# Kernel optimization log

Measured on AMD Instinct MI355X. Metric: run time of the kernel, lower is better.

The kernel has to match this reference:

```python
import jax, jax.numpy as jnp
import numpy as np

N_NODES = 100000
N_EDGES = 1600000
IN_DIM, HID, OUT = 128, 128, 64


def setup_inputs() -> dict:
    key = jax.random.key(0)
    ks = jax.random.split(key, 8)
    x = jax.random.normal(ks[0], (N_NODES, IN_DIM), dtype=jnp.float32)
    edge_index = jax.random.randint(ks[1], (2, N_EDGES), 0, N_NODES, dtype=jnp.int64)
    # Glorot-ish init for GCNConv linear weights (stored as [in, out]).
    W1 = jax.random.normal(ks[2], (IN_DIM, HID), dtype=jnp.float32) * (1.0 / np.sqrt(IN_DIM))
    b1 = jnp.zeros((HID,), dtype=jnp.float32)
    W2 = jax.random.normal(ks[3], (HID, HID), dtype=jnp.float32) * (1.0 / np.sqrt(HID))
    b2 = jnp.zeros((HID,), dtype=jnp.float32)
    W3 = jax.random.normal(ks[4], (HID, OUT), dtype=jnp.float32) * (1.0 / np.sqrt(HID))
    b3 = jnp.zeros((OUT,), dtype=jnp.float32)
    return {"x": x, "W1": W1, "b1": b1, "W2": W2, "b2": b2,
            "W3": W3, "b3": b3, "edge_index": edge_index}


def _gcn_norm(edge_index, num_nodes):
    # GCNConv default: add self loops, symmetric normalization D^{-1/2} A D^{-1/2}.
    loops = jnp.arange(num_nodes, dtype=edge_index.dtype)
    src = jnp.concatenate([edge_index[0], loops])
    dst = jnp.concatenate([edge_index[1], loops])
    deg = jax.ops.segment_sum(jnp.ones_like(dst, dtype=jnp.float32), dst,
                              num_segments=num_nodes)
    dinv = jnp.where(deg > 0, jax.lax.rsqrt(deg), 0.0)
    norm = dinv[src] * dinv[dst]  # [E + N]
    return src, dst, norm


def _gcn_conv(h, W, b, src, dst, norm, num_nodes):
    h = h @ W                                   # transform first (PyG GCNConv)
    msg = h[src] * norm[:, None]                # gather + scale
    agg = jax.ops.segment_sum(msg, dst, num_segments=num_nodes)  # scatter-add
    return agg + b


def _dropout(h, key, p=0.5):
    keep = jax.random.bernoulli(key, 1.0 - p, h.shape)
    return jnp.where(keep, h / (1.0 - p), 0.0)


def reference(x, W1, b1, W2, b2, W3, b3, edge_index):
    num_nodes = x.shape[0]
    src, dst, norm = _gcn_norm(edge_index, num_nodes)
    kd1, kd2 = jax.random.split(jax.random.key(42))
    h = jax.nn.relu(_gcn_conv(x, W1, b1, src, dst, norm, num_nodes))
    h = _dropout(h, kd1)
    h = jax.nn.relu(_gcn_conv(h, W2, b2, src, dst, norm, num_nodes))
    h = _dropout(h, kd2)
    return _gcn_conv(h, W3, b3, src, dst, norm, num_nodes)
```

## Files before the change

### kernel.cpp

```cpp
#include <hip/hip_runtime.h>
#include <stdint.h>

#define NN 100000
#define NE 1600000
#define NMASKW 400000

typedef float f4 __attribute__((ext_vector_type(4)));
typedef float f2 __attribute__((ext_vector_type(2)));
typedef unsigned short us4 __attribute__((ext_vector_type(4)));
typedef short s16x8 __attribute__((ext_vector_type(8)));

__device__ inline float bf2f(unsigned short u) {
  return __uint_as_float(((uint32_t)u) << 16);
}
__device__ inline unsigned short f2bf(float f) {
  uint32_t u = __float_as_uint(f);
  return (unsigned short)((u + 0x7fffu + ((u >> 16) & 1u)) >> 16);
}
__device__ inline float lo16(uint32_t q) { return __uint_as_float(q << 16); }
__device__ inline float hi16(uint32_t q) { return __uint_as_float(q & 0xffff0000u); }

__host__ __device__ inline void threefry2x32(uint32_t k0, uint32_t k1,
                                             uint32_t x0, uint32_t x1,
                                             uint32_t* y0, uint32_t* y1) {
  uint32_t ks[3] = {k0, k1, k0 ^ k1 ^ 0x1BD11BDAu};
  x0 += ks[0]; x1 += ks[1];
  const uint32_t R[2][4] = {{13u, 15u, 26u, 6u}, {17u, 29u, 16u, 24u}};
#pragma unroll
  for (int i = 0; i < 5; ++i) {
#pragma unroll
    for (int j = 0; j < 4; ++j) {
      uint32_t r = R[i & 1][j];
      x0 += x1;
      x1 = (x1 << r) | (x1 >> (32u - r));
      x1 ^= x0;
    }
    x0 += ks[(i + 1) % 3];
    x1 += ks[(i + 2) % 3] + (uint32_t)(i + 1);
  }
  *y0 = x0; *y1 = x1;
}

__device__ inline uint32_t tf_bits32(uint32_t k0, uint32_t k1, uint32_t idx) {
  uint32_t a, b;
  threefry2x32(k0, k1, 0u, idx, &a, &b);
  return a ^ b;
}

__global__ __launch_bounds__(256) void k_mask(uint32_t* __restrict__ m1,
                                              uint32_t* __restrict__ m2,
                                              uint32_t k10, uint32_t k11,
                                              uint32_t k20, uint32_t k21) {
  int t = blockIdx.x * 256 + threadIdx.x;
  if (t >= NMASKW) return;
  uint32_t base = (uint32_t)t * 32u;
  uint32_t w1 = 0, w2 = 0;
#pragma unroll 4
  for (int j = 0; j < 32; ++j) {
    w1 |= (tf_bits32(k10, k11, base + j) >> 31) << j;
    w2 |= (tf_bits32(k20, k21, base + j) >> 31) << j;
  }
  m1[t] = w1;
  m2[t] = w2;
}

__global__ void k_init(uint32_t* cnt) {
  int i = blockIdx.x * 256 + threadIdx.x;
  if (i < NN) cnt[i] = 0u;
}

__global__ void k_hist(const int* __restrict__ ei, uint32_t* __restrict__ cnt,
                       int* __restrict__ slot) {
  int e = blockIdx.x * 256 + threadIdx.x;
  if (e < NE) {
    int d = ei[NE + e];
    slot[e] = (int)atomicAdd(&cnt[d], 1u);
  }
}

__global__ void k_dinv(const uint32_t* __restrict__ cnt, float* __restrict__ dinv) {
  int i = blockIdx.x * 256 + threadIdx.x;
  if (i < NN) dinv[i] = 1.0f / sqrtf((float)(cnt[i] + 1u));
}

__global__ __launch_bounds__(256) void k_scan1(const uint32_t* __restrict__ cnt,
                                               uint32_t* __restrict__ rp,
                                               uint32_t* __restrict__ bsum) {
  __shared__ uint32_t sh[256];
  int t = threadIdx.x;
  int base = blockIdx.x * 1024 + t * 4;
  uint32_t v[4];
  uint32_t s = 0;
#pragma unroll
  for (int i = 0; i < 4; ++i) {
    int idx = base + i;
    v[i] = (idx < NN) ? cnt[idx] : 0u;
    s += v[i];
  }
  sh[t] = s;
  __syncthreads();
  for (int off = 1; off < 256; off <<= 1) {
    uint32_t x = sh[t];
    if (t >= off) x += sh[t - off];
    __syncthreads();
    sh[t] = x;
    __syncthreads();
  }
  uint32_t run = (t > 0) ? sh[t - 1] : 0u;
  if (t == 255) bsum[blockIdx.x] = sh[255];
#pragma unroll
  for (int i = 0; i < 4; ++i) {
    int idx = base + i;
    if (idx < NN) rp[idx] = run;
    run += v[i];
  }
}

__global__ void k_scan2(uint32_t* bsum, int nb) {
  if (threadIdx.x == 0 && blockIdx.x == 0) {
    uint32_t s = 0;
    for (int i = 0; i < nb; ++i) { uint32_t x = bsum[i]; bsum[i] = s; s += x; }
  }
}

__global__ void k_scan3(uint32_t* rp, const uint32_t* __restrict__ bsum) {
  int i = blockIdx.x * 256 + threadIdx.x;
  if (i < NN) rp[i] += bsum[i >> 10];
  if (i == 0) rp[NN] = (uint32_t)NE;
}

__global__ void k_scatter(const int* __restrict__ ei,
                          const uint32_t* __restrict__ rp,
                          const int* __restrict__ slot,
                          const float* __restrict__ dinv,
                          uint2* __restrict__ e2) {
  int e = blockIdx.x * 256 + threadIdx.x;
  if (e < NE) {
    int s = ei[e];
    int d = ei[NE + e];
    float w = dinv[s] * dinv[d];
    uint32_t pos = rp[d] + (uint32_t)slot[e];
    uint2 rec;
    rec.x = (uint32_t)s;
    rec.y = __float_as_uint(w);
    e2[pos] = rec;
  }
}

__global__ void k_wsplit(const float* __restrict__ W, int dout,
                         unsigned short* __restrict__ H,
                         unsigned short* __restrict__ L) {
  int lane = threadIdx.x;
  int kk = blockIdx.x & 3;
  int ct = blockIdx.x >> 2;
  int kbase = kk * 32 + (lane >> 4) * 8;
  int col = ct * 16 + (lane & 15);
  us4 h0, h1, l0, l1;
#pragma unroll
  for (int j = 0; j < 4; ++j) {
    float v = W[(size_t)(kbase + j) * dout + col];
    h0[j] = f2bf(v);
    l0[j] = f2bf(v - bf2f(h0[j]));
    float v2 = W[(size_t)(kbase + 4 + j) * dout + col];
    h1[j] = f2bf(v2);
    l1[j] = f2bf(v2 - bf2f(h1[j]));
  }
  size_t o = ((size_t)blockIdx.x * 64 + lane) * 8;
  *(us4*)(H + o) = h0; *(us4*)(H + o + 4) = h1;
  *(us4*)(L + o) = l0; *(us4*)(L + o + 4) = l1;
}

__global__ __launch_bounds__(256) void k_gemm1(
    const float* __restrict__ A, const unsigned short* __restrict__ Wh,
    const unsigned short* __restrict__ Wl, unsigned short* __restrict__ C) {
  constexpr int NT = 8;
  const int w = threadIdx.x >> 6;
  const int lane = threadIdx.x & 63;
  const int row0 = blockIdx.x * 64 + w * 16;
  int ar = row0 + (lane & 15);
  if (ar >= NN) ar = NN - 1;
  const int aoff = (lane >> 4) * 8;
  s16x8 afh[4], afl[4];
#pragma unroll
  for (int kk = 0; kk < 4; ++kk) {
    f4 v0 = *(const f4*)(A + (size_t)ar * 128 + kk * 32 + aoff);
    f4 v1 = *(const f4*)(A + (size_t)ar * 128 + kk * 32 + aoff + 4);
#pragma unroll
    for (int j = 0; j < 4; ++j) {
      unsigned short h = f2bf(v0[j]);
      afh[kk][j] = (short)h;
      afl[kk][j] = (short)f2bf(v0[j] - bf2f(h));
      unsigned short h2 = f2bf(v1[j]);
      afh[kk][j + 4] = (short)h2;
      afl[kk][j + 4] = (short)f2bf(v1[j] - bf2f(h2));
    }
  }
  f4 acc[NT];
#pragma unroll
  for (int t = 0; t < NT; ++t) acc[t] = (f4){0.f, 0.f, 0.f, 0.f};
#pragma unroll
  for (int ct = 0; ct < NT; ++ct) {
#pragma unroll
    for (int kk = 0; kk < 4; ++kk) {
      size_t bo = ((size_t)(ct * 4 + kk) * 64 + lane) * 8;
      s16x8 bh = *(const s16x8*)(Wh + bo);
      s16x8 bl = *(const s16x8*)(Wl + bo);
      acc[ct] = __builtin_amdgcn_mfma_f32_16x16x32_bf16(afh[kk], bh, acc[ct], 0, 0, 0);
      acc[ct] = __builtin_amdgcn_mfma_f32_16x16x32_bf16(afh[kk], bl, acc[ct], 0, 0, 0);
      acc[ct] = __builtin_amdgcn_mfma_f32_16x16x32_bf16(afl[kk], bh, acc[ct], 0, 0, 0);
    }
  }
  const int rbase = row0 + (lane >> 4) * 4;
  const int cbase = lane & 15;
#pragma unroll
  for (int ct = 0; ct < NT; ++ct) {
#pragma unroll
    for (int r = 0; r < 4; ++r) {
      int gr = rbase + r;
      if (gr < NN) C[(size_t)gr * 128 + ct * 16 + cbase] = f2bf(acc[ct][r]);
    }
  }
}

template <int DOUT>
__global__ __launch_bounds__(256) void k_gemm_mfma(
    const unsigned short* __restrict__ Ah, const unsigned short* __restrict__ Al,
    const unsigned short* __restrict__ Wh, const unsigned short* __restrict__ Wl,
    unsigned short* __restrict__ C) {
  constexpr int NT = DOUT / 16;
  const int w = threadIdx.x >> 6;
  const int lane = threadIdx.x & 63;
  const int row0 = blockIdx.x * 64 + w * 16;
  int ar = row0 + (lane & 15);
  if (ar >= NN) ar = NN - 1;
  const int aoff = (lane >> 4) * 8;
  s16x8 afh[4], afl[4];
#pragma unroll
  for (int kk = 0; kk < 4; ++kk) {
    afh[kk] = *(const s16x8*)(Ah + (size_t)ar * 128 + kk * 32 + aoff);
    afl[kk] = *(const s16x8*)(Al + (size_t)ar * 128 + kk * 32 + aoff);
  }
  f4 acc[NT];
#pragma unroll
  for (int t = 0; t < NT; ++t) acc[t] = (f4){0.f, 0.f, 0.f, 0.f};
#pragma unroll
  for (int ct = 0; ct < NT; ++ct) {
#pragma unroll
    for (int kk = 0; kk < 4; ++kk) {
      size_t bo = ((size_t)(ct * 4 + kk) * 64 + lane) * 8;
      s16x8 bh = *(const s16x8*)(Wh + bo);
      s16x8 bl = *(const s16x8*)(Wl + bo);
      acc[ct] = __builtin_amdgcn_mfma_f32_16x16x32_bf16(afh[kk], bh, acc[ct], 0, 0, 0);
      acc[ct] = __builtin_amdgcn_mfma_f32_16x16x32_bf16(afh[kk], bl, acc[ct], 0, 0, 0);
      acc[ct] = __builtin_amdgcn_mfma_f32_16x16x32_bf16(afl[kk], bh, acc[ct], 0, 0, 0);
    }
  }
  const int rbase = row0 + (lane >> 4) * 4;
  const int cbase = lane & 15;
#pragma unroll
  for (int ct = 0; ct < NT; ++ct) {
#pragma unroll
    for (int r = 0; r < 4; ++r) {
      int gr = rbase + r;
      if (gr < NN) C[(size_t)gr * DOUT + ct * 16 + cbase] = f2bf(acc[ct][r]);
    }
  }
}

__global__ __launch_bounds__(256) void k_agg_mid(
    const unsigned short* __restrict__ hb, const uint32_t* __restrict__ rp,
    const uint2* __restrict__ e2, const float* __restrict__ dinv,
    const float* __restrict__ bias, const uint32_t* __restrict__ mask,
    unsigned short* __restrict__ oh, unsigned short* __restrict__ ol) {
  int wid = __builtin_amdgcn_readfirstlane(blockIdx.x * 4 + (threadIdx.x >> 6));
  if (wid >= NN) return;
  const int lane = threadIdx.x & 63;
  const uint32_t beg = rp[wid], end = rp[wid + 1];
  const float dv = dinv[wid];
  const float sn = dv * dv;
  const char* hbase = (const char*)hb;
  float a0 = 0.f, a1 = 0.f, c0 = 0.f, c1 = 0.f;
  uint32_t u = beg;
  for (; u + 8 <= end; u += 8) {
    uint2 r[8];
#pragma unroll
    for (int i = 0; i < 8; ++i) r[i] = e2[u + i];
    uint32_t q[8];
#pragma unroll
    for (int i = 0; i < 8; ++i)
      q[i] = ((const uint32_t*)(hbase + ((size_t)r[i].x << 8)))[lane];
#pragma unroll
    for (int i = 0; i < 8; ++i) {
      float w = __uint_as_float(r[i].y);
      if (i & 1) {
        c0 = fmaf(w, lo16(q[i]), c0);
        c1 = fmaf(w, hi16(q[i]), c1);
      } else {
        a0 = fmaf(w, lo16(q[i]), a0);
        a1 = fmaf(w, hi16(q[i]), a1);
      }
    }
  }
  for (; u < end; ++u) {
    uint2 r = e2[u];
    uint32_t q = ((const uint32_t*)(hbase + ((size_t)r.x << 8)))[lane];
    float w = __uint_as_float(r.y);
    a0 = fmaf(w, lo16(q), a0);
    a1 = fmaf(w, hi16(q), a1);
  }
  a0 += c0; a1 += c1;
  uint32_t qs = ((const uint32_t*)(hbase + ((size_t)(uint32_t)wid << 8)))[lane];
  f2 bv = *(const f2*)(bias + lane * 2);
  a0 = fmaf(sn, lo16(qs), a0) + bv[0];
  a1 = fmaf(sn, hi16(qs), a1) + bv[1];
  a0 = fmaxf(a0, 0.f);
  a1 = fmaxf(a1, 0.f);
  uint32_t mw = mask[(uint32_t)wid * 4u + (uint32_t)(lane >> 4)];
  uint32_t b = (uint32_t)((lane & 15) * 2);
  a0 = ((mw >> b) & 1u) ? 0.f : a0 * 2.f;
  a1 = ((mw >> (b + 1u)) & 1u) ? 0.f : a1 * 2.f;
  unsigned short h0 = f2bf(a0), h1 = f2bf(a1);
  unsigned short g0 = f2bf(a0 - bf2f(h0)), g1 = f2bf(a1 - bf2f(h1));
  ((uint32_t*)oh)[(size_t)wid * 64 + lane] = (uint32_t)h0 | ((uint32_t)h1 << 16);
  ((uint32_t*)ol)[(size_t)wid * 64 + lane] = (uint32_t)g0 | ((uint32_t)g1 << 16);
}

__global__ __launch_bounds__(256) void k_agg_final(
    const unsigned short* __restrict__ hb, const uint32_t* __restrict__ rp,
    const uint2* __restrict__ e2, const float* __restrict__ dinv,
    const float* __restrict__ bias, float* __restrict__ out) {
  int wid = __builtin_amdgcn_readfirstlane(blockIdx.x * 4 + (threadIdx.x >> 6));
  if (wid >= NN) return;
  const int lane = threadIdx.x & 63;
  const uint32_t beg = rp[wid], end = rp[wid + 1];
  const float dv = dinv[wid];
  const float sn = dv * dv;
  const char* hbase = (const char*)hb;
  float a0 = 0.f, c0 = 0.f, a2 = 0.f, c2 = 0.f;
  uint32_t u = beg;
  for (; u + 8 <= end; u += 8) {
    uint2 r[8];
#pragma unroll
    for (int i = 0; i < 8; ++i) r[i] = e2[u + i];
    uint32_t q[8];
#pragma unroll
    for (int i = 0; i < 8; ++i)
      q[i] = (uint32_t)((const unsigned short*)(hbase + ((size_t)r[i].x << 7)))[lane];
#pragma unroll
    for (int i = 0; i < 8; ++i) {
      float w = __uint_as_float(r[i].y);
      float hv = __uint_as_float(q[i] << 16);
      if ((i & 3) == 0) a0 = fmaf(w, hv, a0);
      else if ((i & 3) == 1) c0 = fmaf(w, hv, c0);
      else if ((i & 3) == 2) a2 = fmaf(w, hv, a2);
      else c2 = fmaf(w, hv, c2);
    }
  }
  for (; u < end; ++u) {
    uint2 r = e2[u];
    uint32_t q = (uint32_t)((const unsigned short*)(hbase + ((size_t)r.x << 7)))[lane];
    a0 = fmaf(__uint_as_float(r.y), __uint_as_float(q << 16), a0);
  }
  a0 += c0 + a2 + c2;
  uint32_t qs = (uint32_t)((const unsigned short*)(hbase + ((size_t)(uint32_t)wid << 7)))[lane];
  a0 = fmaf(sn, __uint_as_float(qs << 16), a0) + bias[lane];
  out[(size_t)wid * 64 + lane] = a0;
}

extern "C" void kernel_launch(void* const* d_in, const int* in_sizes, int n_in,
                              void* d_out, int out_size, void* d_ws, size_t ws_size,
                              hipStream_t stream) {
  (void)in_sizes; (void)n_in; (void)out_size; (void)ws_size;
  const float* x  = (const float*)d_in[0];
  const float* W1 = (const float*)d_in[1];
  const float* b1 = (const float*)d_in[2];
  const float* W2 = (const float*)d_in[3];
  const float* b2 = (const float*)d_in[4];
  const float* W3 = (const float*)d_in[5];
  const float* b3 = (const float*)d_in[6];
  const int* ei   = (const int*)d_in[7];
  float* out = (float*)d_out;

  char* p = (char*)d_ws;
  auto alloc = [&](size_t bytes) -> void* {
    void* r = (void*)p;
    p += (bytes + 255) & ~(size_t)255;
    return r;
  };
  uint32_t* cnt  = (uint32_t*)alloc((size_t)NN * 4);
  float*    dinv = (float*)alloc((size_t)NN * 4);
  uint32_t* rp   = (uint32_t*)alloc((size_t)(NN + 1) * 4);
  uint32_t* bsum = (uint32_t*)alloc(1024);
  int*      slot = (int*)alloc((size_t)NE * 4);
  uint2*    e2   = (uint2*)alloc((size_t)NE * 8);
  uint32_t* m1   = (uint32_t*)alloc((size_t)NMASKW * 4);
  uint32_t* m2   = (uint32_t*)alloc((size_t)NMASKW * 4);
  unsigned short* ah = (unsigned short*)alloc((size_t)NN * 128 * 2);
  unsigned short* al = (unsigned short*)alloc((size_t)NN * 128 * 2);
  unsigned short* hb = (unsigned short*)alloc((size_t)NN * 128 * 2);
  unsigned short* w1h = (unsigned short*)alloc(32 * 64 * 8 * 2);
  unsigned short* w1l = (unsigned short*)alloc(32 * 64 * 8 * 2);
  unsigned short* w2h = (unsigned short*)alloc(32 * 64 * 8 * 2);
  unsigned short* w2l = (unsigned short*)alloc(32 * 64 * 8 * 2);
  unsigned short* w3h = (unsigned short*)alloc(16 * 64 * 8 * 2);
  unsigned short* w3l = (unsigned short*)alloc(16 * 64 * 8 * 2);

  uint32_t kd1a, kd1b, kd2a, kd2b;
  threefry2x32(0u, 42u, 0u, 0u, &kd1a, &kd1b);
  threefry2x32(0u, 42u, 0u, 1u, &kd2a, &kd2b);

  const int gbN = (NN + 255) / 256;
  const int gbE = (NE + 255) / 256;
  const int gbScan = (NN + 1023) / 1024;
  const int gbGemm = (NN + 63) / 64;
  const int gbAgg = (NN + 3) / 4;
  const int gbMask = (NMASKW + 255) / 256;

  k_init<<<gbN, 256, 0, stream>>>(cnt);
  k_hist<<<gbE, 256, 0, stream>>>(ei, cnt, slot);
  k_dinv<<<gbN, 256, 0, stream>>>(cnt, dinv);
  k_scan1<<<gbScan, 256, 0, stream>>>(cnt, rp, bsum);
  k_scan2<<<1, 64, 0, stream>>>(bsum, gbScan);
  k_scan3<<<gbN, 256, 0, stream>>>(rp, bsum);
  k_scatter<<<gbE, 256, 0, stream>>>(ei, rp, slot, dinv, e2);

  k_mask<<<gbMask, 256, 0, stream>>>(m1, m2, kd1a, kd1b, kd2a, kd2b);
  k_wsplit<<<32, 64, 0, stream>>>(W1, 128, w1h, w1l);
  k_wsplit<<<32, 64, 0, stream>>>(W2, 128, w2h, w2l);
  k_wsplit<<<16, 64, 0, stream>>>(W3, 64, w3h, w3l);

  k_gemm1<<<gbGemm, 256, 0, stream>>>(x, w1h, w1l, hb);
  k_agg_mid<<<gbAgg, 256, 0, stream>>>(hb, rp, e2, dinv, b1, m1, ah, al);
  k_gemm_mfma<128><<<gbGemm, 256, 0, stream>>>(ah, al, w2h, w2l, hb);
  k_agg_mid<<<gbAgg, 256, 0, stream>>>(hb, rp, e2, dinv, b2, m2, ah, al);
  k_gemm_mfma<64><<<gbGemm, 256, 0, stream>>>(ah, al, w3h, w3l, hb);
  k_agg_final<<<gbAgg, 256, 0, stream>>>(hb, rp, e2, dinv, b3, out);
}
```

Measured before the change: 440.9 us.

## Fuse setup kernels and split edges across quarter-waves in aggregation

Merges the histogram and dropout-mask kernels into one interleaved launch, folds dinv into the scan, replaces the init kernel with a memset, and merges the three weight-split launches into one. The aggregation kernels now handle four edges at once per wave, with each 16-lane group doing 16-byte row gathers, followed by a cross-group shuffle reduction. This cuts launch count and issues fewer, wider gathers per edge. The cost is shuffle reduction overhead and padded tail iterations for nodes with low degree.

```diff
diff --git a/kernel.cpp b/kernel.cpp
--- a/kernel.cpp
+++ b/kernel.cpp
@@ -4,6 +4,8 @@
 #define NN 100000
 #define NE 1600000
 #define NMASKW 400000
+#define GB_E 6250
+#define GB_MASK 1563
 
 typedef float f4 __attribute__((ext_vector_type(4)));
 typedef float f2 __attribute__((ext_vector_type(2)));
@@ -47,45 +49,38 @@
   return a ^ b;
 }
 
-__global__ __launch_bounds__(256) void k_mask(uint32_t* __restrict__ m1,
-                                              uint32_t* __restrict__ m2,
-                                              uint32_t k10, uint32_t k11,
-                                              uint32_t k20, uint32_t k21) {
-  int t = blockIdx.x * 256 + threadIdx.x;
-  if (t >= NMASKW) return;
-  uint32_t base = (uint32_t)t * 32u;
-  uint32_t w1 = 0, w2 = 0;
+__global__ __launch_bounds__(256) void k_histmask(
+    const int* __restrict__ ei, uint32_t* __restrict__ cnt,
+    int* __restrict__ slot, uint32_t* __restrict__ m1, uint32_t* __restrict__ m2,
+    uint32_t k10, uint32_t k11, uint32_t k20, uint32_t k21) {
+  int b = blockIdx.x;
+  int q = b / 5, r = b % 5;
+  if (r < 4) {
+    int e = (q * 4 + r) * 256 + threadIdx.x;
+    if (e < NE) {
+      int d = ei[NE + e];
+      slot[e] = (int)atomicAdd(&cnt[d], 1u);
+    }
+  } else {
+    int t = q * 256 + threadIdx.x;
+    if (t < NMASKW) {
+      uint32_t base = (uint32_t)t * 32u;
+      uint32_t w1 = 0, w2 = 0;
 #pragma unroll 4
-  for (int j = 0; j < 32; ++j) {
-    w1 |= (tf_bits32(k10, k11, base + j) >> 31) << j;
-    w2 |= (tf_bits32(k20, k21, base + j) >> 31) << j;
-  }
-  m1[t] = w1;
-  m2[t] = w2;
-}
-
-__global__ void k_init(uint32_t* cnt) {
-  int i = blockIdx.x * 256 + threadIdx.x;
-  if (i < NN) cnt[i] = 0u;
-}
-
-__global__ void k_hist(const int* __restrict__ ei, uint32_t* __restrict__ cnt,
-                       int* __restrict__ slot) {
-  int e = blockIdx.x * 256 + threadIdx.x;
-  if (e < NE) {
-    int d = ei[NE + e];
-    slot[e] = (int)atomicAdd(&cnt[d], 1u);
-  }
-}
-
-__global__ void k_dinv(const uint32_t* __restrict__ cnt, float* __restrict__ dinv) {
-  int i = blockIdx.x * 256 + threadIdx.x;
-  if (i < NN) dinv[i] = 1.0f / sqrtf((float)(cnt[i] + 1u));
+      for (int j = 0; j < 32; ++j) {
+        w1 |= (tf_bits32(k10, k11, base + j) >> 31) << j;
+        w2 |= (tf_bits32(k20, k21, base + j) >> 31) << j;
+      }
+      m1[t] = w1;
+      m2[t] = w2;
+    }
+  }
 }
 
 __global__ __launch_bounds__(256) void k_scan1(const uint32_t* __restrict__ cnt,
                                                uint32_t* __restrict__ rp,
-                                               uint32_t* __restrict__ bsum) {
+                                               uint32_t* __restrict__ bsum,
+                                               float* __restrict__ dinv) {
   __shared__ uint32_t sh[256];
   int t = threadIdx.x;
   int base = blockIdx.x * 1024 + t * 4;
@@ -95,6 +90,7 @@
   for (int i = 0; i < 4; ++i) {
     int idx = base + i;
     v[i] = (idx < NN) ? cnt[idx] : 0u;
+    if (idx < NN) dinv[idx] = 1.0f / sqrtf((float)(v[i] + 1u));
     s += v[i];
   }
   sh[t] = s;
@@ -147,12 +143,19 @@
   }
 }
 
-__global__ void k_wsplit(const float* __restrict__ W, int dout,
-                         unsigned short* __restrict__ H,
-                         unsigned short* __restrict__ L) {
+__global__ void k_wsplit3(const float* __restrict__ W1, const float* __restrict__ W2,
+                          const float* __restrict__ W3,
+                          unsigned short* __restrict__ w1h, unsigned short* __restrict__ w1l,
+                          unsigned short* __restrict__ w2h, unsigned short* __restrict__ w2l,
+                          unsigned short* __restrict__ w3h, unsigned short* __restrict__ w3l) {
+  int b = blockIdx.x;
+  const float* W; unsigned short *H, *L; int dout, bb;
+  if (b < 32)      { W = W1; H = w1h; L = w1l; dout = 128; bb = b; }
+  else if (b < 64) { W = W2; H = w2h; L = w2l; dout = 128; bb = b - 32; }
+  else             { W = W3; H = w3h; L = w3l; dout = 64;  bb = b - 64; }
   int lane = threadIdx.x;
-  int kk = blockIdx.x & 3;
-  int ct = blockIdx.x >> 2;
+  int kk = bb & 3;
+  int ct = bb >> 2;
   int kbase = kk * 32 + (lane >> 4) * 8;
   int col = ct * 16 + (lane & 15);
   us4 h0, h1, l0, l1;
@@ -165,7 +168,7 @@
     h1[j] = f2bf(v2);
     l1[j] = f2bf(v2 - bf2f(h1[j]));
   }
-  size_t o = ((size_t)blockIdx.x * 64 + lane) * 8;
+  size_t o = ((size_t)bb * 64 + lane) * 8;
   *(us4*)(H + o) = h0; *(us4*)(H + o + 4) = h1;
   *(us4*)(L + o) = l0; *(us4*)(L + o + 4) = l1;
 }
@@ -275,54 +278,82 @@
   int wid = __builtin_amdgcn_readfirstlane(blockIdx.x * 4 + (threadIdx.x >> 6));
   if (wid >= NN) return;
   const int lane = threadIdx.x & 63;
+  const int q = lane >> 4;
+  const int fl = lane & 15;
   const uint32_t beg = rp[wid], end = rp[wid + 1];
   const float dv = dinv[wid];
   const float sn = dv * dv;
   const char* hbase = (const char*)hb;
-  float a0 = 0.f, a1 = 0.f, c0 = 0.f, c1 = 0.f;
+  float acc[8];
+#pragma unroll
+  for (int j = 0; j < 8; ++j) acc[j] = 0.f;
+
   uint32_t u = beg;
   for (; u + 8 <= end; u += 8) {
-    uint2 r[8];
-#pragma unroll
-    for (int i = 0; i < 8; ++i) r[i] = e2[u + i];
-    uint32_t q[8];
-#pragma unroll
-    for (int i = 0; i < 8; ++i)
-      q[i] = ((const uint32_t*)(hbase + ((size_t)r[i].x << 8)))[lane];
-#pragma unroll
-    for (int i = 0; i < 8; ++i) {
-      float w = __uint_as_float(r[i].y);
-      if (i & 1) {
-        c0 = fmaf(w, lo16(q[i]), c0);
-        c1 = fmaf(w, hi16(q[i]), c1);
-      } else {
-        a0 = fmaf(w, lo16(q[i]), a0);
-        a1 = fmaf(w, hi16(q[i]), a1);
-      }
-    }
-  }
-  for (; u < end; ++u) {
-    uint2 r = e2[u];
-    uint32_t q = ((const uint32_t*)(hbase + ((size_t)r.x << 8)))[lane];
-    float w = __uint_as_float(r.y);
-    a0 = fmaf(w, lo16(q), a0);
-    a1 = fmaf(w, hi16(q), a1);
-  }
-  a0 += c0; a1 += c1;
-  uint32_t qs = ((const uint32_t*)(hbase + ((size_t)(uint32_t)wid << 8)))[lane];
-  f2 bv = *(const f2*)(bias + lane * 2);
-  a0 = fmaf(sn, lo16(qs), a0) + bv[0];
-  a1 = fmaf(sn, hi16(qs), a1) + bv[1];
-  a0 = fmaxf(a0, 0.f);
-  a1 = fmaxf(a1, 0.f);
-  uint32_t mw = mask[(uint32_t)wid * 4u + (uint32_t)(lane >> 4)];
-  uint32_t b = (uint32_t)((lane & 15) * 2);
-  a0 = ((mw >> b) & 1u) ? 0.f : a0 * 2.f;
-  a1 = ((mw >> (b + 1u)) & 1u) ? 0.f : a1 * 2.f;
-  unsigned short h0 = f2bf(a0), h1 = f2bf(a1);
-  unsigned short g0 = f2bf(a0 - bf2f(h0)), g1 = f2bf(a1 - bf2f(h1));
-  ((uint32_t*)oh)[(size_t)wid * 64 + lane] = (uint32_t)h0 | ((uint32_t)h1 << 16);
-  ((uint32_t*)ol)[(size_t)wid * 64 + lane] = (uint32_t)g0 | ((uint32_t)g1 << 16);
+    uint2 r0 = e2[u + q];
+    uint2 r1 = e2[u + 4 + q];
+    uint4 g0 = *(const uint4*)(hbase + ((size_t)r0.x << 8) + fl * 16);
+    uint4 g1 = *(const uint4*)(hbase + ((size_t)r1.x << 8) + fl * 16);
+    float w0 = __uint_as_float(r0.y), w1 = __uint_as_float(r1.y);
+    acc[0] = fmaf(w0, lo16(g0.x), acc[0]); acc[1] = fmaf(w0, hi16(g0.x), acc[1]);
+    acc[2] = fmaf(w0, lo16(g0.y), acc[2]); acc[3] = fmaf(w0, hi16(g0.y), acc[3]);
+    acc[4] = fmaf(w0, lo16(g0.z), acc[4]); acc[5] = fmaf(w0, hi16(g0.z), acc[5]);
+    acc[6] = fmaf(w0, lo16(g0.w), acc[6]); acc[7] = fmaf(w0, hi16(g0.w), acc[7]);
+    acc[0] = fmaf(w1, lo16(g1.x), acc[0]); acc[1] = fmaf(w1, hi16(g1.x), acc[1]);
+    acc[2] = fmaf(w1, lo16(g1.y), acc[2]); acc[3] = fmaf(w1, hi16(g1.y), acc[3]);
+    acc[4] = fmaf(w1, lo16(g1.z), acc[4]); acc[5] = fmaf(w1, hi16(g1.z), acc[5]);
+    acc[6] = fmaf(w1, lo16(g1.w), acc[6]); acc[7] = fmaf(w1, hi16(g1.w), acc[7]);
+  }
+  for (; u < end; u += 4) {
+    uint32_t idx = u + (uint32_t)q;
+    uint32_t cidx = idx < end ? idx : end - 1u;
+    uint2 r = e2[cidx];
+    float w = (idx < end) ? __uint_as_float(r.y) : 0.f;
+    uint4 g = *(const uint4*)(hbase + ((size_t)r.x << 8) + fl * 16);
+    acc[0] = fmaf(w, lo16(g.x), acc[0]); acc[1] = fmaf(w, hi16(g.x), acc[1]);
+    acc[2] = fmaf(w, lo16(g.y), acc[2]); acc[3] = fmaf(w, hi16(g.y), acc[3]);
+    acc[4] = fmaf(w, lo16(g.z), acc[4]); acc[5] = fmaf(w, hi16(g.z), acc[5]);
+    acc[6] = fmaf(w, lo16(g.w), acc[6]); acc[7] = fmaf(w, hi16(g.w), acc[7]);
+  }
+#pragma unroll
+  for (int j = 0; j < 8; ++j) acc[j] += __shfl_xor(acc[j], 16);
+#pragma unroll
+  for (int j = 0; j < 8; ++j) acc[j] += __shfl_xor(acc[j], 32);
+
+  uint4 qs = *(const uint4*)(hbase + ((size_t)(uint32_t)wid << 8) + fl * 16);
+  f4 b0 = *(const f4*)(bias + fl * 8);
+  f4 b1 = *(const f4*)(bias + fl * 8 + 4);
+  acc[0] = fmaf(sn, lo16(qs.x), acc[0]) + b0[0];
+  acc[1] = fmaf(sn, hi16(qs.x), acc[1]) + b0[1];
+  acc[2] = fmaf(sn, lo16(qs.y), acc[2]) + b0[2];
+  acc[3] = fmaf(sn, hi16(qs.y), acc[3]) + b0[3];
+  acc[4] = fmaf(sn, lo16(qs.z), acc[4]) + b1[0];
+  acc[5] = fmaf(sn, hi16(qs.z), acc[5]) + b1[1];
+  acc[6] = fmaf(sn, lo16(qs.w), acc[6]) + b1[2];
+  acc[7] = fmaf(sn, hi16(qs.w), acc[7]) + b1[3];
+  uint32_t mw = mask[(uint32_t)wid * 4u + (uint32_t)(fl >> 2)];
+  uint32_t bb = (uint32_t)((fl & 3) * 8);
+#pragma unroll
+  for (int j = 0; j < 8; ++j) {
+    float a = fmaxf(acc[j], 0.f);
+    acc[j] = ((mw >> (bb + j)) & 1u) ? 0.f : a * 2.f;
+  }
+  uint32_t hw[4], lw[4];
+#pragma unroll
+  for (int j = 0; j < 4; ++j) {
+    unsigned short h0 = f2bf(acc[2 * j]), h1 = f2bf(acc[2 * j + 1]);
+    unsigned short g0 = f2bf(acc[2 * j] - bf2f(h0));
+    unsigned short g1 = f2bf(acc[2 * j + 1] - bf2f(h1));
+    hw[j] = (uint32_t)h0 | ((uint32_t)h1 << 16);
+    lw[j] = (uint32_t)g0 | ((uint32_t)g1 << 16);
+  }
+  if (q == 0) {
+    uint4 v = {hw[0], hw[1], hw[2], hw[3]};
+    *(uint4*)(oh + (size_t)(uint32_t)wid * 128 + fl * 8) = v;
+  } else if (q == 1) {
+    uint4 v = {lw[0], lw[1], lw[2], lw[3]};
+    *(uint4*)(ol + (size_t)(uint32_t)wid * 128 + fl * 8) = v;
+  }
 }
 
 __global__ __launch_bounds__(256) void k_agg_final(
@@ -332,39 +363,52 @@
   int wid = __builtin_amdgcn_readfirstlane(blockIdx.x * 4 + (threadIdx.x >> 6));
   if (wid >= NN) return;
   const int lane = threadIdx.x & 63;
+  const int q = lane >> 4;
+  const int fl = lane & 15;
   const uint32_t beg = rp[wid], end = rp[wid + 1];
   const float dv = dinv[wid];
   const float sn = dv * dv;
   const char* hbase = (const char*)hb;
-  float a0 = 0.f, c0 = 0.f, a2 = 0.f, c2 = 0.f;
+  float acc[4];
+#pragma unroll
+  for (int j = 0; j < 4; ++j) acc[j] = 0.f;
+
   uint32_t u = beg;
   for (; u + 8 <= end; u += 8) {
-    uint2 r[8];
-#pragma unroll
-    for (int i = 0; i < 8; ++i) r[i] = e2[u + i];
-    uint32_t q[8];
-#pragma unroll
-    for (int i = 0; i < 8; ++i)
-      q[i] = (uint32_t)((const unsigned short*)(hbase + ((size_t)r[i].x << 7)))[lane];
-#pragma unroll
-    for (int i = 0; i < 8; ++i) {
-      float w = __uint_as_float(r[i].y);
-      float hv = __uint_as_float(q[i] << 16);
-      if ((i & 3) == 0) a0 = fmaf(w, hv, a0);
-      else if ((i & 3) == 1) c0 = fmaf(w, hv, c0);
-      else if ((i & 3) == 2) a2 = fmaf(w, hv, a2);
-      else c2 = fmaf(w, hv, c2);
-    }
-  }
-  for (; u < end; ++u) {
-    uint2 r = e2[u];
-    uint32_t q = (uint32_t)((const unsigned short*)(hbase + ((size_t)r.x << 7)))[lane];
-    a0 = fmaf(__uint_as_float(r.y), __uint_as_float(q << 16), a0);
-  }
-  a0 += c0 + a2 + c2;
-  uint32_t qs = (uint32_t)((const unsigned short*)(hbase + ((size_t)(uint32_t)wid << 7)))[lane];
-  a0 = fmaf(sn, __uint_as_float(qs << 16), a0) + bias[lane];
-  out[(size_t)wid * 64 + lane] = a0;
+    uint2 r0 = e2[u + q];
+    uint2 r1 = e2[u + 4 + q];
+    uint2 g0 = *(const uint2*)(hbase + ((size_t)r0.x << 7) + fl * 8);
+    uint2 g1 = *(const uint2*)(hbase + ((size_t)r1.x << 7) + fl * 8);
+    float w0 = __uint_as_float(r0.y), w1 = __uint_as_float(r1.y);
+    acc[0] = fmaf(w0, lo16(g0.x), acc[0]); acc[1] = fmaf(w0, hi16(g0.x), acc[1]);
+    acc[2] = fmaf(w0, lo16(g0.y), acc[2]); acc[3] = fmaf(w0, hi16(g0.y), acc[3]);
+    acc[0] = fmaf(w1, lo16(g1.x), acc[0]); acc[1] = fmaf(w1, hi16(g1.x), acc[1]);
+    acc[2] = fmaf(w1, lo16(g1.y), acc[2]); acc[3] = fmaf(w1, hi16(g1.y), acc[3]);
+  }
+  for (; u < end; u += 4) {
+    uint32_t idx = u + (uint32_t)q;
+    uint32_t cidx = idx < end ? idx : end - 1u;
+    uint2 r = e2[cidx];
+    float w = (idx < end) ? __uint_as_float(r.y) : 0.f;
+    uint2 g = *(const uint2*)(hbase + ((size_t)r.x << 7) + fl * 8);
+    acc[0] = fmaf(w, lo16(g.x), acc[0]); acc[1] = fmaf(w, hi16(g.x), acc[1]);
+    acc[2] = fmaf(w, lo16(g.y), acc[2]); acc[3] = fmaf(w, hi16(g.y), acc[3]);
+  }
+#pragma unroll
+  for (int j = 0; j < 4; ++j) acc[j] += __shfl_xor(acc[j], 16);
+#pragma unroll
+  for (int j = 0; j < 4; ++j) acc[j] += __shfl_xor(acc[j], 32);
+
+  uint2 qs = *(const uint2*)(hbase + ((size_t)(uint32_t)wid << 7) + fl * 8);
+  f4 bv = *(const f4*)(bias + fl * 4);
+  acc[0] = fmaf(sn, lo16(qs.x), acc[0]) + bv[0];
+  acc[1] = fmaf(sn, hi16(qs.x), acc[1]) + bv[1];
+  acc[2] = fmaf(sn, lo16(qs.y), acc[2]) + bv[2];
+  acc[3] = fmaf(sn, hi16(qs.y), acc[3]) + bv[3];
+  if (q == 0) {
+    f4 v = {acc[0], acc[1], acc[2], acc[3]};
+    *(f4*)(out + (size_t)(uint32_t)wid * 64 + fl * 4) = v;
+  }
 }
 
 extern "C" void kernel_launch(void* const* d_in, const int* in_sizes, int n_in,
@@ -414,20 +458,14 @@
   const int gbScan = (NN + 1023) / 1024;
   const int gbGemm = (NN + 63) / 64;
   const int gbAgg = (NN + 3) / 4;
-  const int gbMask = (NMASKW + 255) / 256;
-
-  k_init<<<gbN, 256, 0, stream>>>(cnt);
-  k_hist<<<gbE, 256, 0, stream>>>(ei, cnt, slot);
-  k_dinv<<<gbN, 256, 0, stream>>>(cnt, dinv);
-  k_scan1<<<gbScan, 256, 0, stream>>>(cnt, rp, bsum);
+
+  hipMemsetAsync(cnt, 0, (size_t)NN * 4, stream);
+  k_histmask<<<8000, 256, 0, stream>>>(ei, cnt, slot, m1, m2, kd1a, kd1b, kd2a, kd2b);
+  k_scan1<<<gbScan, 256, 0, stream>>>(cnt, rp, bsum, dinv);
   k_scan2<<<1, 64, 0, stream>>>(bsum, gbScan);
   k_scan3<<<gbN, 256, 0, stream>>>(rp, bsum);
   k_scatter<<<gbE, 256, 0, stream>>>(ei, rp, slot, dinv, e2);
-
-  k_mask<<<gbMask, 256, 0, stream>>>(m1, m2, kd1a, kd1b, kd2a, kd2b);
-  k_wsplit<<<32, 64, 0, stream>>>(W1, 128, w1h, w1l);
-  k_wsplit<<<32, 64, 0, stream>>>(W2, 128, w2h, w2l);
-  k_wsplit<<<16, 64, 0, stream>>>(W3, 64, w3h, w3l);
+  k_wsplit3<<<80, 64, 0, stream>>>(W1, W2, W3, w1h, w1l, w2h, w2l, w3h, w3l);
 
   k_gemm1<<<gbGemm, 256, 0, stream>>>(x, w1h, w1l, hb);
   k_agg_mid<<<gbAgg, 256, 0, stream>>>(hb, rp, e2, dinv, b1, m1, ah, al);
```

Measured after the change: 398.3 us. -9.7%, faster.
